# Kernel optimization log

Hardware: AMD Instinct MI355X
Metric: run time of the kernel (lower is better)

## Reference

```python
import jax, jax.numpy as jnp
import numpy as np
from jax import lax

VOCAB, EMBED, HIDDEN, TAGS, PAD = 50000, 512, 512, 20, 0
B, T = 64, 512


def _lstm_layer(xs, W_ih, W_hh, b_ih, b_hh):
    # xs: (B, T, D) -> hs: (B, T, H). PyTorch ifgo gate order.
    Bm = xs.shape[0]
    H = W_hh.shape[1]
    h0 = jnp.zeros((Bm, H), xs.dtype)
    c0 = jnp.zeros((Bm, H), xs.dtype)
    # precompute input projections for all timesteps: (T, B, 4H)
    xproj = jnp.einsum('btd,gd->tbg', xs, W_ih) + b_ih

    def step(carry, xp_t):
        h, c = carry
        gates = xp_t + h @ W_hh.T + b_hh
        i, f, g, o = jnp.split(gates, 4, axis=-1)
        i = jax.nn.sigmoid(i)
        f = jax.nn.sigmoid(f)
        g = jnp.tanh(g)
        o = jax.nn.sigmoid(o)
        c = f * c + i * g
        h = o * jnp.tanh(c)
        return (h, c), h

    (_, _), hs = lax.scan(step, (h0, c0), xproj)
    return hs.transpose(1, 0, 2)  # (B, T, H)


def setup_inputs() -> dict:
    key = jax.random.key(0)
    ks = jax.random.split(key, 12)
    s = 0.05
    emb = jax.random.normal(ks[0], (VOCAB, EMBED), jnp.float32) * s
    emb = emb.at[PAD].set(0.0)  # padding_idx row is zero
    W_ih0 = jax.random.normal(ks[1], (4 * HIDDEN, EMBED), jnp.float32) * s
    W_hh0 = jax.random.normal(ks[2], (4 * HIDDEN, HIDDEN), jnp.float32) * s
    b_ih0 = jax.random.normal(ks[3], (4 * HIDDEN,), jnp.float32) * s
    b_hh0 = jax.random.normal(ks[4], (4 * HIDDEN,), jnp.float32) * s
    W_ih1 = jax.random.normal(ks[5], (4 * HIDDEN, HIDDEN), jnp.float32) * s
    W_hh1 = jax.random.normal(ks[6], (4 * HIDDEN, HIDDEN), jnp.float32) * s
    b_ih1 = jax.random.normal(ks[7], (4 * HIDDEN,), jnp.float32) * s
    b_hh1 = jax.random.normal(ks[8], (4 * HIDDEN,), jnp.float32) * s
    W_out = jax.random.normal(ks[9], (TAGS, HIDDEN), jnp.float32) * s
    b_out = jax.random.normal(ks[10], (TAGS,), jnp.float32) * s
    x = jax.random.randint(ks[11], (B, T), 0, VOCAB, dtype=jnp.int64 if jax.config.jax_enable_x64 else jnp.int32)
    return dict(x=x, emb=emb, W_ih0=W_ih0, W_hh0=W_hh0, b_ih0=b_ih0, b_hh0=b_hh0,
                W_ih1=W_ih1, W_hh1=W_hh1, b_ih1=b_ih1, b_hh1=b_hh1,
                W_out=W_out, b_out=b_out)


def reference(x, emb, W_ih0, W_hh0, b_ih0, b_hh0, W_ih1, W_hh1, b_ih1, b_hh1, W_out, b_out):
    batch_size, max_len = x.shape
    lens = max_len - jnp.sum(x == PAD, axis=-1)  # (B,)
    h = emb[x]                                    # (B, T, E) embedding lookup
    h = _lstm_layer(h, W_ih0, W_hh0, b_ih0, b_hh0)
    h = _lstm_layer(h, W_ih1, W_hh1, b_ih1, b_hh1)
    last = h[jnp.arange(batch_size), lens - 1, :]  # length-masked last-step gather
    return last @ W_out.T + b_out                  # (B, TAGS)
```

## Files before the change

### kernel.cpp

```cpp
#include <hip/hip_runtime.h>
#include <hip/hip_bf16.h>
#include <stdint.h>

#define B_    64
#define T_    512
#define H_    512
#define G_    2048
#define TAGS_ 20

typedef __hip_bfloat16 bf16;
typedef __bf16 bf16x8 __attribute__((ext_vector_type(8)));
typedef float  f32x4  __attribute__((ext_vector_type(4)));
typedef unsigned int u32;
typedef u32 u32x4 __attribute__((ext_vector_type(4)));
typedef u32 u32x2 __attribute__((ext_vector_type(2)));

__device__ __forceinline__ float sigmoidf_(float x) { return 1.0f / (1.0f + __expf(-x)); }
__device__ __forceinline__ float tanhf_(float x)    { return 1.0f - 2.0f / (__expf(2.0f * x) + 1.0f); }


__global__ void k_zero(uint32_t* __restrict__ p, int n) {
    for (int i = blockIdx.x * blockDim.x + threadIdx.x; i < n; i += gridDim.x * blockDim.x)
        p[i] = 0u;
}

__global__ void k_addb(const float* __restrict__ a, const float* __restrict__ b,
                       float* __restrict__ o, int n) {
    for (int i = blockIdx.x * blockDim.x + threadIdx.x; i < n; i += gridDim.x * blockDim.x)
        o[i] = a[i] + b[i];
}

__global__ __launch_bounds__(256) void k_lens(const int* __restrict__ x, int* __restrict__ lens) {
    int b = blockIdx.x;
    int cnt = 0;
    for (int tpos = threadIdx.x; tpos < T_; tpos += 256)
        cnt += (x[(size_t)b * T_ + tpos] == 0) ? 1 : 0;
    #pragma unroll
    for (int off = 32; off; off >>= 1) cnt += __shfl_xor(cnt, off);
    __shared__ int tot;
    if (threadIdx.x == 0) tot = 0;
    __syncthreads();
    if ((threadIdx.x & 63) == 0) atomicAdd(&tot, cnt);
    __syncthreads();
    if (threadIdx.x == 0) lens[b] = T_ - tot;
}

__global__ __launch_bounds__(256) void k_gather(const int* __restrict__ x,
                                                const float* __restrict__ emb,
                                                char* __restrict__ Epk) {
    const int t = blockIdx.x, m = blockIdx.y;
    __shared__ int tok[16];
    if (threadIdx.x < 16) tok[threadIdx.x] = x[(size_t)(m * 16 + threadIdx.x) * T_ + t];
    __syncthreads();
    char* base = Epk + ((size_t)(t * 4 + m)) * 16384;
    for (int task = threadIdx.x; task < 1024; task += 256) {
        int f = task >> 6, lane = task & 63;
        int r = lane & 15, kqi = lane >> 4;
        const float* src = emb + (size_t)tok[r] * H_ + f * 32 + kqi * 8;
        bf16 tmp[8];
        #pragma unroll
        for (int e = 0; e < 8; ++e) tmp[e] = __float2bfloat16(src[e]);
        *reinterpret_cast<f32x4*>(base + f * 1024 + lane * 16) =
            *reinterpret_cast<f32x4*>(tmp);
    }
}

__global__ __launch_bounds__(256) void k_pack(const float* __restrict__ Wih0, const float* __restrict__ Whh0,
                                              const float* __restrict__ Wih1, const float* __restrict__ Whh1,
                                              bf16* __restrict__ Wp) {
    const int s = blockIdx.x, q = blockIdx.y, l = blockIdx.z;
    const float* Wx = l ? Wih1 : Wih0;
    const float* Wh = l ? Whh1 : Whh0;
    bf16* base = Wp + (size_t)(l * 32 + s) * 65536;
    for (int u = threadIdx.x; u < 2048; u += 256) {
        int kc = u >> 6, lane = u & 63;
        int row = q * H_ + s * 16 + (lane & 15);
        int col = (kc & 15) * 32 + (lane >> 4) * 8;
        const float* src = ((kc < 16) ? Wx : Wh) + (size_t)row * H_ + col;
        bf16* dst = base + ((size_t)(q * 32 + kc) * 64 + lane) * 8;
        #pragma unroll
        for (int e = 0; e < 8; ++e) dst[e] = __float2bfloat16(src[e]);
    }
}


#define WAITALL()                                                            \
    asm volatile("s_waitcnt vmcnt(0)" ::: "memory");                         \
    __builtin_amdgcn_sched_barrier(0);

#define ISSUE_CHF(CA, CB, base, SC)                                          \
    _Pragma("unroll")                                                        \
    for (int i = 0; i < 4; ++i) {                                            \
        const char* pa_ = (base) + (2 * (q * 4 + i) + (kqi >> 1)) * 1024     \
                          + (qa * 16 + row) * 16;                            \
        asm volatile("global_load_dwordx4 %0, %2, off" SC "\n\t"             \
                     "global_load_dwordx4 %1, %3, off" SC                    \
                     : "=v"(CA[i]), "=v"(CB[i])                              \
                     : "v"(pa_), "v"(pa_ + 256));                            \
    }

#define CHECK8(CA, CB, sq, okv)                                              \
    { okv = 1;                                                               \
      _Pragma("unroll")                                                      \
      for (int i = 0; i < 4; ++i)                                            \
          okv &= (CA[i].z == (u32)(sq)) & (CB[i].z == (u32)(sq)); }

#define STAGE_CH(CA, CB, fbase)                                              \
    _Pragma("unroll")                                                        \
    for (int i = 0; i < 4; ++i) {                                            \
        u32x4 fr_ = u32x4{CA[i].x, CA[i].y, CB[i].x, CB[i].y};               \
        stagev[(size_t)((fbase) + q * 4 + i) * 64 + lane] =                  \
            __builtin_bit_cast(f32x4, fr_);                                  \
    }

#define ISSUE16L(arr, basep)                                                 \
    _Pragma("unroll")                                                        \
    for (int kc = 0; kc < 16; ++kc) {                                        \
        asm volatile("global_load_dwordx4 %0, %1, off"                       \
                     : "=v"(arr[kc]) : "v"((basep) + kc * 1024));            \
    }

#define MFMA16_REG(arr, woff)                                                \
    _Pragma("unroll")                                                        \
    for (int kc = 0; kc < 16; ++kc) {                                        \
        f32x4 wf = wldsv[(size_t)(q * 32 + (woff) + kc) * 64 + lane];        \
        acc[kc & 3] = __builtin_amdgcn_mfma_f32_16x16x32_bf16(               \
            __builtin_bit_cast(bf16x8, arr[kc]),                             \
            __builtin_bit_cast(bf16x8, wf), acc[kc & 3], 0, 0, 0);           \
    }

#define MFMA16_S(soff, woff)                                                 \
    _Pragma("unroll")                                                        \
    for (int kc = 0; kc < 16; ++kc) {                                        \
        f32x4 af = stagev[(size_t)((soff) + kc) * 64 + lane];                \
        f32x4 wf = wldsv[(size_t)(q * 32 + (woff) + kc) * 64 + lane];        \
        acc[kc & 3] = __builtin_amdgcn_mfma_f32_16x16x32_bf16(               \
            __builtin_bit_cast(bf16x8, af),                                  \
            __builtin_bit_cast(bf16x8, wf), acc[kc & 3], 0, 0, 0);           \
    }

__global__ __launch_bounds__(256, 1) void k_lstm(
    const bf16* __restrict__ Wp, const char* __restrict__ Epk,
    const float* __restrict__ bias0, const float* __restrict__ bias1,
    char* __restrict__ h0ring, char* __restrict__ h1ring,
    char* __restrict__ h0loc, char* __restrict__ h1loc,
    int* __restrict__ fx, float* __restrict__ last1, const int* __restrict__ lens)
{
    extern __shared__ char smem[];
    f32x4* wldsv  = (f32x4*)smem;
    f32x4* stagev = (f32x4*)(smem + 131072);

    const int bid   = blockIdx.x;
    const int g     = bid & 7;
    const int s     = bid >> 3;
    const int layer = g >> 2;
    const int m     = g & 3;
    const int tid   = threadIdx.x;
    const int lane  = tid & 63;
    const int q     = tid >> 6;
    const int kqi   = lane >> 4;
    const int row   = lane & 15;
    const int qa    = (kqi & 1) * 2;

    float (*glds)[16][20] = layer ? (float (*)[16][20])(smem + 131072)
                                  : (float (*)[16][20])(smem + 131072 + 16384);
    bf16* hlds = layer ? (bf16*)(smem + 131072 + 5120)
                       : (bf16*)(smem + 131072 + 16384 + 5120);

    {
        const f32x4* wsrc = (const f32x4*)(Wp + (size_t)(layer * 32 + s) * 65536);
        for (int i = tid; i < 8192; i += 256) wldsv[i] = wsrc[i];
    }

    const int eb   = tid >> 4;
    const int ej   = tid & 15;
    const int brow = m * 16 + eb;
    const int jcol = s * 16 + ej;
    float c_reg = 0.f;
    const float* bias = layer ? bias1 : bias0;
    const float bi0 = bias[0 * H_ + jcol];
    const float bi1 = bias[1 * H_ + jcol];
    const float bi2 = bias[2 * H_ + jcol];
    const float bi3 = bias[3 * H_ + jcol];
    int target = lens[brow] - 1;
    if (target < 0) target = T_ - 1;

    int* flagp = fx + m * 32;

    char* grp0 = h0ring + (size_t)m * 8 * 32768;
    char* grp1 = h1ring + (size_t)m * 8 * 32768;
    char* loc0 = h0loc + (size_t)m * 8 * 32768;
    char* loc1 = h1loc + (size_t)m * 8 * 32768;
    char* mygrp = layer ? grp1 : grp0;
    char* myloc = layer ? loc1 : loc0;
    const int rb = (lane >> 4) * 4;
    const int l15 = lane & 15;

    __syncthreads();

    for (int tt = 0; tt < T_; ++tt) {
        f32x4 acc[4];
        #pragma unroll
        for (int i = 0; i < 4; ++i) acc[i] = f32x4{0.f, 0.f, 0.f, 0.f};
        const int slot_w = tt & 7;
        const int slot_r = (tt - 1) & 7;

        if (layer == 0) {
            f32x4 xreg[16];
            const char* xp = Epk + ((size_t)(tt * 4 + m)) * 16384 + lane * 16;
            ISSUE16L(xreg, xp)
            const char* hL = loc0 + slot_r * 32768;
            const char* hG = grp0 + slot_r * 32768;
            u32x4 ca[4], cb[4];
            ISSUE_CHF(ca, cb, hL, " sc0")
            WAITALL()
            MFMA16_REG(xreg, 0)
            int ok; CHECK8(ca, cb, tt, ok)
            int gd = 0;
            while (!__all(ok)) {
                if (++gd > (1 << 16)) break;
                u32x4 ga[4], gb[4];
                ISSUE_CHF(ca, cb, hL, " sc0")
                ISSUE_CHF(ga, gb, hG, " sc0 sc1")
                WAITALL()
                CHECK8(ca, cb, tt, ok)
                if (!__all(ok)) {
                    int ok2; CHECK8(ga, gb, tt, ok2)
                    if (__all(ok2)) {
                        #pragma unroll
                        for (int i = 0; i < 4; ++i) { ca[i] = ga[i]; cb[i] = gb[i]; }
                        ok = 1;
                    }
                }
            }
            __builtin_amdgcn_sched_barrier(0);
            STAGE_CH(ca, cb, 0)
            __syncthreads();
            MFMA16_S(0, 16)
        } else {
            const char* xG = grp0 + slot_w * 32768;
            const char* hL = loc1 + slot_r * 32768;
            const char* hG = grp1 + slot_r * 32768;
            u32x4 xa[4], xb[4], ha[4], hb[4];
            ISSUE_CHF(ha, hb, hL, " sc0")
            ISSUE_CHF(xa, xb, xG, " sc0 sc1")
            WAITALL()
            int okx, okh;
            CHECK8(xa, xb, tt + 1, okx)
            CHECK8(ha, hb, tt, okh)
            int gd = 0;
            while (!__all(okx & okh)) {
                if (++gd > (1 << 16)) break;
                if (!__all(okh)) {
                    u32x4 ga[4], gb[4];
                    ISSUE_CHF(ha, hb, hL, " sc0")
                    ISSUE_CHF(ga, gb, hG, " sc0 sc1")
                    WAITALL()
                    CHECK8(ha, hb, tt, okh)
                    if (!__all(okh)) {
                        int ok2; CHECK8(ga, gb, tt, ok2)
                        if (__all(ok2)) {
                            #pragma unroll
                            for (int i = 0; i < 4; ++i) { ha[i] = ga[i]; hb[i] = gb[i]; }
                            okh = 1;
                        }
                    }
                }
                if (!__all(okx)) {
                    ISSUE_CHF(xa, xb, xG, " sc0 sc1")
                    WAITALL()
                    CHECK8(xa, xb, tt + 1, okx)
                }
            }
            __builtin_amdgcn_sched_barrier(0);
            STAGE_CH(xa, xb, 0)
            STAGE_CH(ha, hb, 16)
            __syncthreads();
            if (tid == 0) {
                int fv = tt + 1;
                asm volatile("global_store_dword %0, %1, off sc0 sc1" :: "v"(flagp), "v"(fv) : "memory");
            }
            MFMA16_S(0, 0)
            MFMA16_S(16, 16)
            __syncthreads();
        }

        f32x4 gsum = (acc[0] + acc[1]) + (acc[2] + acc[3]);

        *reinterpret_cast<f32x4*>(&glds[q][l15][rb]) = gsum;
        __syncthreads();

        float gi = sigmoidf_(glds[0][ej][eb] + bi0);
        float gf = sigmoidf_(glds[1][ej][eb] + bi1);
        float gg = tanhf_  (glds[2][ej][eb] + bi2);
        float go = sigmoidf_(glds[3][ej][eb] + bi3);
        c_reg = gf * c_reg + gi * gg;
        float hn = go * tanhf_(c_reg);

        hlds[eb * 16 + ej] = __float2bfloat16(hn);
        if (layer == 1 && tt == target)
            last1[(size_t)brow * H_ + jcol] = hn;
        __syncthreads();

        if (layer == 0 && tid < 64 && tt >= 8) {
            int gd2 = 0;
            while (true) {
                int v;
                asm volatile("global_load_dword %0, %1, off sc0 sc1\n\ts_waitcnt vmcnt(0)"
                             : "=v"(v) : "v"(flagp) : "memory");
                if (v >= tt - 7) break;
                if (++gd2 > (1 << 16)) break;
                __builtin_amdgcn_s_sleep(2);
            }
            __builtin_amdgcn_sched_barrier(0);
        }

        if (tid < 64) {
            int prow = tid & 15, pq = tid >> 4;
            u32x2 d = *reinterpret_cast<const u32x2*>(&hlds[prow * 16 + pq * 4]);
            u32x4 ch = u32x4{d.x, d.y, (u32)(tt + 1), 0u};
            f32x4 chv = __builtin_bit_cast(f32x4, ch);
            char* dstL = myloc + slot_w * 32768 + s * 1024 + tid * 16;
            char* dstG = mygrp + slot_w * 32768 + s * 1024 + tid * 16;
            asm volatile("global_store_dwordx4 %0, %1, off sc0"
                         :: "v"(dstL), "v"(chv) : "memory");
            asm volatile("global_store_dwordx4 %0, %1, off sc0 sc1"
                         :: "v"(dstG), "v"(chv) : "memory");
        }
    }
}

__global__ __launch_bounds__(64) void k_out(const float* __restrict__ last1,
                                            const float* __restrict__ Wout,
                                            const float* __restrict__ bout,
                                            float* __restrict__ out) {
    int b = blockIdx.x, tg = blockIdx.y, lane = threadIdx.x;
    float sum = 0.f;
    for (int d = lane; d < H_; d += 64)
        sum += last1[(size_t)b * H_ + d] * Wout[(size_t)tg * H_ + d];
    #pragma unroll
    for (int off = 32; off; off >>= 1) sum += __shfl_xor(sum, off);
    if (lane == 0) out[b * TAGS_ + tg] = sum + bout[tg];
}


extern "C" void kernel_launch(void* const* d_in, const int* in_sizes, int n_in,
                              void* d_out, int out_size, void* d_ws, size_t ws_size,
                              hipStream_t stream)
{
    const int*   x    = (const int*)  d_in[0];
    const float* emb  = (const float*)d_in[1];
    const float* Wih0 = (const float*)d_in[2];
    const float* Whh0 = (const float*)d_in[3];
    const float* bih0 = (const float*)d_in[4];
    const float* bhh0 = (const float*)d_in[5];
    const float* Wih1 = (const float*)d_in[6];
    const float* Whh1 = (const float*)d_in[7];
    const float* bih1 = (const float*)d_in[8];
    const float* bhh1 = (const float*)d_in[9];
    const float* Wout = (const float*)d_in[10];
    const float* bout = (const float*)d_in[11];
    float* out = (float*)d_out;

    char* p = (char*)d_ws;
    char* Epk  = p;         p += (size_t)T_ * 4 * 16384;
    bf16* Wp   = (bf16*)p;  p += (size_t)2 * 32 * 65536 * 2;
    float* bias0 = (float*)p; p += (size_t)G_ * 4;
    float* bias1 = (float*)p; p += (size_t)G_ * 4;
    char* zbase = p;
    char* h0ring = p; p += (size_t)4 * 8 * 32768;
    char* h1ring = p; p += (size_t)4 * 8 * 32768;
    char* h0loc  = p; p += (size_t)4 * 8 * 32768;
    char* h1loc  = p; p += (size_t)4 * 8 * 32768;
    int*  fx     = (int*)p;  p += 8 * 32 * 4;
    size_t zbytes = (size_t)(p - zbase);
    float* last1 = (float*)p; p += (size_t)B_ * H_ * 4;
    int* lens = (int*)p; p += 256;

    (void)hipFuncSetAttribute((const void*)k_lstm,
                              hipFuncAttributeMaxDynamicSharedMemorySize, 163840);

    k_zero<<<dim3(128), dim3(256), 0, stream>>>((uint32_t*)zbase, (int)(zbytes / 4));
    k_lens<<<dim3(B_), dim3(256), 0, stream>>>(x, lens);
    k_addb<<<dim3(8), dim3(256), 0, stream>>>(bih0, bhh0, bias0, G_);
    k_addb<<<dim3(8), dim3(256), 0, stream>>>(bih1, bhh1, bias1, G_);
    k_pack<<<dim3(32, 4, 2), dim3(256), 0, stream>>>(Wih0, Whh0, Wih1, Whh1, Wp);
    k_gather<<<dim3(T_, 4), dim3(256), 0, stream>>>(x, emb, Epk);

    k_lstm<<<dim3(256), dim3(256), 163840, stream>>>(Wp, Epk, bias0, bias1,
                                                     h0ring, h1ring, h0loc, h1loc,
                                                     fx, last1, lens);

    k_out<<<dim3(B_, TAGS_), dim3(64), 0, stream>>>(last1, Wout, bout, out);
}
```

Measured before the change: 1.468 ms.

## Permute packed weight rows so gate math stays in registers via lane shuffles

The packed weight layout is reordered so each wave's MFMA output tile holds all four gates for its own hidden columns. A cross-lane shuffle butterfly then brings i/f/g/o together in each lane, so the LDS gate exchange and two barriers per timestep go away, and the h chunk is packed with shuffles and stored straight from 16 lanes per wave. This shortens the serial per-step critical path of the recurrent loop. In exchange it adds one barrier before staging to protect LDS reuse, plus extra shuffle instructions, and it depends on the new weight packing matching the MFMA output mapping exactly.

```diff
diff --git a/kernel.cpp b/kernel.cpp
--- a/kernel.cpp
+++ b/kernel.cpp
@@ -74,7 +74,8 @@
     bf16* base = Wp + (size_t)(l * 32 + s) * 65536;
     for (int u = threadIdx.x; u < 2048; u += 256) {
         int kc = u >> 6, lane = u & 63;
-        int row = q * H_ + s * 16 + (lane & 15);
+        int c = lane & 15;
+        int row = (c & 3) * H_ + s * 16 + q * 4 + (c >> 2);
         int col = (kc & 15) * 32 + (lane >> 4) * 8;
         const float* src = ((kc < 16) ? Wx : Wh) + (size_t)row * H_ + col;
         bf16* dst = base + ((size_t)(q * 32 + kc) * 64 + lane) * 8;
@@ -162,20 +163,15 @@
     const int row   = lane & 15;
     const int qa    = (kqi & 1) * 2;
 
-    float (*glds)[16][20] = layer ? (float (*)[16][20])(smem + 131072)
-                                  : (float (*)[16][20])(smem + 131072 + 16384);
-    bf16* hlds = layer ? (bf16*)(smem + 131072 + 5120)
-                       : (bf16*)(smem + 131072 + 16384 + 5120);
-
     {
         const f32x4* wsrc = (const f32x4*)(Wp + (size_t)(layer * 32 + s) * 65536);
         for (int i = tid; i < 8192; i += 256) wldsv[i] = wsrc[i];
     }
 
-    const int eb   = tid >> 4;
-    const int ej   = tid & 15;
-    const int brow = m * 16 + eb;
-    const int jcol = s * 16 + ej;
+    const int jj    = (lane >> 2) & 3;
+    const int b_loc = 4 * (lane >> 4) + (lane & 3);
+    const int brow  = m * 16 + b_loc;
+    const int jcol  = s * 16 + q * 4 + jj;
     float c_reg = 0.f;
     const float* bias = layer ? bias1 : bias0;
     const float bi0 = bias[0 * H_ + jcol];
@@ -193,8 +189,6 @@
     char* loc1 = h1loc + (size_t)m * 8 * 32768;
     char* mygrp = layer ? grp1 : grp0;
     char* myloc = layer ? loc1 : loc0;
-    const int rb = (lane >> 4) * 4;
-    const int l15 = lane & 15;
 
     __syncthreads();
 
@@ -234,6 +228,7 @@
                 }
             }
             __builtin_amdgcn_sched_barrier(0);
+            __syncthreads();
             STAGE_CH(ca, cb, 0)
             __syncthreads();
             MFMA16_S(0, 16)
@@ -273,6 +268,7 @@
                 }
             }
             __builtin_amdgcn_sched_barrier(0);
+            __syncthreads();
             STAGE_CH(xa, xb, 0)
             STAGE_CH(ha, hb, 16)
             __syncthreads();
@@ -282,50 +278,62 @@
             }
             MFMA16_S(0, 0)
             MFMA16_S(16, 16)
-            __syncthreads();
         }
 
-        f32x4 gsum = (acc[0] + acc[1]) + (acc[2] + acc[3]);
-
-        *reinterpret_cast<f32x4*>(&glds[q][l15][rb]) = gsum;
-        __syncthreads();
-
-        float gi = sigmoidf_(glds[0][ej][eb] + bi0);
-        float gf = sigmoidf_(glds[1][ej][eb] + bi1);
-        float gg = tanhf_  (glds[2][ej][eb] + bi2);
-        float go = sigmoidf_(glds[3][ej][eb] + bi3);
+        f32x4 v = (acc[0] + acc[1]) + (acc[2] + acc[3]);
+
+        float r0 = __shfl_xor(v.x, 1), r1 = __shfl_xor(v.y, 1),
+              r2 = __shfl_xor(v.z, 1), r3 = __shfl_xor(v.w, 1);
+        const bool oddl = (lane & 1) != 0;
+        float n0 = oddl ? r1 : v.x;
+        float n1 = oddl ? v.y : r0;
+        float n2 = oddl ? r3 : v.z;
+        float n3 = oddl ? v.w : r2;
+        float s0 = __shfl_xor(n0, 2), s1 = __shfl_xor(n1, 2),
+              s2 = __shfl_xor(n2, 2), s3 = __shfl_xor(n3, 2);
+        const bool hil = (lane & 2) != 0;
+        float mi = hil ? s2 : n0;
+        float mf = hil ? s3 : n1;
+        float mg = hil ? n2 : s0;
+        float mo = hil ? n3 : s1;
+
+        float gi = sigmoidf_(mi + bi0);
+        float gf = sigmoidf_(mf + bi1);
+        float gg = tanhf_  (mg + bi2);
+        float go = sigmoidf_(mo + bi3);
         c_reg = gf * c_reg + gi * gg;
         float hn = go * tanhf_(c_reg);
-
-        hlds[eb * 16 + ej] = __float2bfloat16(hn);
         if (layer == 1 && tt == target)
             last1[(size_t)brow * H_ + jcol] = hn;
-        __syncthreads();
 
         if (layer == 0 && tid < 64 && tt >= 8) {
             int gd2 = 0;
             while (true) {
-                int v;
+                int vfl;
                 asm volatile("global_load_dword %0, %1, off sc0 sc1\n\ts_waitcnt vmcnt(0)"
-                             : "=v"(v) : "v"(flagp) : "memory");
-                if (v >= tt - 7) break;
+                             : "=v"(vfl) : "v"(flagp) : "memory");
+                if (vfl >= tt - 7) break;
                 if (++gd2 > (1 << 16)) break;
                 __builtin_amdgcn_s_sleep(2);
             }
             __builtin_amdgcn_sched_barrier(0);
         }
 
-        if (tid < 64) {
-            int prow = tid & 15, pq = tid >> 4;
-            u32x2 d = *reinterpret_cast<const u32x2*>(&hlds[prow * 16 + pq * 4]);
-            u32x4 ch = u32x4{d.x, d.y, (u32)(tt + 1), 0u};
-            f32x4 chv = __builtin_bit_cast(f32x4, ch);
-            char* dstL = myloc + slot_w * 32768 + s * 1024 + tid * 16;
-            char* dstG = mygrp + slot_w * 32768 + s * 1024 + tid * 16;
-            asm volatile("global_store_dwordx4 %0, %1, off sc0"
-                         :: "v"(dstL), "v"(chv) : "memory");
-            asm volatile("global_store_dwordx4 %0, %1, off sc0 sc1"
-                         :: "v"(dstG), "v"(chv) : "memory");
+        {
+            bf16 hb16 = __float2bfloat16(hn);
+            u32 hw = (u32)__builtin_bit_cast(unsigned short, hb16);
+            u32 p1 = __shfl_xor(hw, 4);
+            u32 w  = (hw & 0xffffu) | (p1 << 16);
+            u32 w2 = __shfl_xor(w, 8);
+            if ((lane & 12) == 0) {
+                u32x4 ch = u32x4{w, w2, (u32)(tt + 1), 0u};
+                f32x4 chv = __builtin_bit_cast(f32x4, ch);
+                size_t off = (size_t)slot_w * 32768 + s * 1024 + (q * 16 + b_loc) * 16;
+                asm volatile("global_store_dwordx4 %0, %1, off sc0"
+                             :: "v"(myloc + off), "v"(chv) : "memory");
+                asm volatile("global_store_dwordx4 %0, %1, off sc0 sc1"
+                             :: "v"(mygrp + off), "v"(chv) : "memory");
+            }
         }
     }
 }
```

New measurement: 1.462 ms (median of 2 runs). No clear change (-0.4%).
